# Performance work log

Measured on AMD Instinct MI355X. Metric: run time of the kernel, lower is better.

## Reference

```python
import jax, jax.numpy as jnp
import numpy as np
import math

IN_CH = 32
OUT_CH = 32
NODE_NUM = 24
BATCH = 32768
# skeleton edges: self-loops + chain (parent -> child), matching init_kwargs
_SRC = list(range(24)) + list(range(23))
_DST = list(range(24)) + list(range(1, 24))


def _build_mask():
    # block mask: block (dst, src) of size [OUT_CH, IN_CH] set to 1 per edge
    m = np.zeros((OUT_CH * NODE_NUM, IN_CH * NODE_NUM), dtype=np.float32)
    for s, d in zip(_SRC, _DST):
        m[OUT_CH * d:OUT_CH * (d + 1), IN_CH * s:IN_CH * (s + 1)] = 1.0
    return jnp.asarray(m)


def setup_inputs() -> dict:
    key = jax.random.key(0)
    kx, kw, kb = jax.random.split(key, 3)
    mask = _build_mask()
    dim = IN_CH * NODE_NUM
    # kaiming-uniform-like per-block init approximated by scaled normal; only
    # values inside mask blocks matter (forward multiplies by mask anyway)
    weight = jax.random.normal(kw, (OUT_CH * NODE_NUM, dim), dtype=jnp.float32) * (1.0 / math.sqrt(IN_CH))
    bound = 1.0 / math.sqrt(dim)
    bias = jax.random.uniform(kb, (OUT_CH * NODE_NUM,), dtype=jnp.float32, minval=-bound, maxval=bound)
    x = jax.random.normal(kx, (BATCH, dim), dtype=jnp.float32)
    return {"x": x, "weight": weight, "bias": bias, "mask": mask}


def reference(x, weight, bias, mask):
    # F.linear(x, weight * mask, bias) == x @ (weight*mask)^T + bias
    w = weight * mask
    return jnp.einsum("bi,oi->bo", x, w) + bias
```

## Files before the change

### kernel.cpp

```cpp
#include <hip/hip_runtime.h>
#include <hip/hip_bf16.h>


typedef __bf16 bf16x8 __attribute__((ext_vector_type(8)));
typedef float  f32x4  __attribute__((ext_vector_type(4)));

#define DIM 768
#define STRIDE 770
#define NFRAG (24 * 2 * 2)

__device__ __forceinline__ bf16x8 cvt8(const float* __restrict__ p) {
    float4 lo = *(const float4*)p;
    float4 hi = *(const float4*)(p + 4);
    bf16x8 r;
    r[0] = (__bf16)lo.x; r[1] = (__bf16)lo.y; r[2] = (__bf16)lo.z; r[3] = (__bf16)lo.w;
    r[4] = (__bf16)hi.x; r[5] = (__bf16)hi.y; r[6] = (__bf16)hi.z; r[7] = (__bf16)hi.w;
    return r;
}

__global__ void prepack_w_kernel(const float* __restrict__ w, bf16x8* __restrict__ ws)
{
    const int fid = blockIdx.x * 256 + threadIdx.x;
    const int lane = fid & 63;
    const int ni   = (fid >> 6) & 1;
    const int kt   = (fid >> 7) & 1;
    const int d    = fid >> 8;
    const int quad = lane >> 4, l16 = lane & 15;

    bf16x8 v;
    if (d == 0 && kt == 0) {
#pragma unroll
        for (int j = 0; j < 8; ++j) v[j] = (__bf16)0.f;
    } else {
        const float* src = w + (long)(32 * d + 16 * ni + l16) * DIM
                             + (32 * d - 32 + 32 * kt + 8 * quad);
        v = cvt8(src);
    }
    ws[fid] = v;
}

__global__ __launch_bounds__(512, 4)
void skeleton_linear_kernel(const float* __restrict__ x,
                            const float* __restrict__ bias,
                            const bf16x8* __restrict__ wfrag,
                            float* __restrict__ out)
{
    __shared__ float lds[16 * STRIDE];

    const int tid  = threadIdx.x;
    const int lane = tid & 63;
    const int wave = tid >> 6;
    const int quad = lane >> 4;
    const int l16  = lane & 15;
    const long row0 = (long)blockIdx.x * 16;

    {
        const float4* gx = (const float4*)(x + row0 * DIM);
        float4 st[6];
#pragma unroll
        for (int i = 0; i < 6; ++i) st[i] = gx[tid + 512 * i];
#pragma unroll
        for (int i = 0; i < 6; ++i) {
            int f = tid + 512 * i;
            int r = f / 192, c4 = f % 192;
            *(float4*)&lds[r * STRIDE + 4 * c4] = st[i];
        }
    }
    __syncthreads();

    f32x4 acc[3][2];
#pragma unroll
    for (int i = 0; i < 3; ++i) {
        const int d = wave * 3 + i;
        f32x4 a0 = {0.f, 0.f, 0.f, 0.f};
        f32x4 a1 = {0.f, 0.f, 0.f, 0.f};
#pragma unroll
        for (int kt = 0; kt < 2; ++kt) {
            int k0 = 32 * d - 32 + 32 * kt + 8 * quad;
            int kA = k0 < 0 ? 0 : k0;
            bf16x8 a = cvt8(&lds[l16 * STRIDE + kA]);
            const int fb = (d * 2 + kt) * 2;
            a0 = __builtin_amdgcn_mfma_f32_16x16x32_bf16(a, wfrag[fb * 64 + lane], a0, 0, 0, 0);
            a1 = __builtin_amdgcn_mfma_f32_16x16x32_bf16(a, wfrag[(fb + 1) * 64 + lane], a1, 0, 0, 0);
        }
        acc[i][0] = a0;
        acc[i][1] = a1;
    }
    __syncthreads();

#pragma unroll
    for (int i = 0; i < 3; ++i) {
        const int d = wave * 3 + i;
#pragma unroll
        for (int ni = 0; ni < 2; ++ni) {
            const float bi = bias[32 * d + 16 * ni + l16];
#pragma unroll
            for (int r = 0; r < 4; ++r)
                lds[(4 * quad + r) * STRIDE + 32 * d + 16 * ni + l16] = acc[i][ni][r] + bi;
        }
    }
    __syncthreads();

    {
        float* go = out + row0 * DIM;
#pragma unroll
        for (int i = 0; i < 6; ++i) {
            int f = tid + 512 * i;
            int r = f / 192, c4 = f % 192;
            float4 v = *(const float4*)&lds[r * STRIDE + 4 * c4];
            *(float4*)(go + (long)r * DIM + 4 * c4) = v;
        }
    }
}

extern "C" void kernel_launch(void* const* d_in, const int* in_sizes, int n_in,
                              void* d_out, int out_size, void* d_ws, size_t ws_size,
                              hipStream_t stream) {
    const float* x    = (const float*)d_in[0];
    const float* w    = (const float*)d_in[1];
    const float* bias = (const float*)d_in[2];
    float* out = (float*)d_out;

    bf16x8* wpack = (bf16x8*)d_ws;

    prepack_w_kernel<<<NFRAG * 64 / 256, 256, 0, stream>>>(w, wpack);

    const int BATCH = 32768;
    dim3 grid(BATCH / 16);
    skeleton_linear_kernel<<<grid, 512, 0, stream>>>(x, bias, wpack, out);
}
```

Baseline: 188.5 us.

## Load x straight into MFMA fragments and store outputs directly without LDS

Drops the LDS staging of x and of the output tile, along with its three block barriers. Each lane now loads its MFMA operand slices straight from global memory. The weight and activation operands are swapped so that each lane's accumulator holds four consecutive output channels, which lets it write a float4 directly to global memory. Bias is added by initialising the accumulators from it. The cost is that global loads and stores are less coalesced per instruction (strided rows, 32-byte and 16-byte chunks), traded for removing LDS traffic and synchronisation.

```diff
diff --git a/kernel.cpp b/kernel.cpp
--- a/kernel.cpp
+++ b/kernel.cpp
@@ -6,12 +6,18 @@
 typedef float  f32x4  __attribute__((ext_vector_type(4)));
 
 #define DIM 768
-#define STRIDE 770
 #define NFRAG (24 * 2 * 2)
 
 __device__ __forceinline__ bf16x8 cvt8(const float* __restrict__ p) {
     float4 lo = *(const float4*)p;
     float4 hi = *(const float4*)(p + 4);
+    bf16x8 r;
+    r[0] = (__bf16)lo.x; r[1] = (__bf16)lo.y; r[2] = (__bf16)lo.z; r[3] = (__bf16)lo.w;
+    r[4] = (__bf16)hi.x; r[5] = (__bf16)hi.y; r[6] = (__bf16)hi.z; r[7] = (__bf16)hi.w;
+    return r;
+}
+
+__device__ __forceinline__ bf16x8 cvt8r(float4 lo, float4 hi) {
     bf16x8 r;
     r[0] = (__bf16)lo.x; r[1] = (__bf16)lo.y; r[2] = (__bf16)lo.z; r[3] = (__bf16)lo.w;
     r[4] = (__bf16)hi.x; r[5] = (__bf16)hi.y; r[6] = (__bf16)hi.z; r[7] = (__bf16)hi.w;
@@ -45,71 +51,40 @@
                             const bf16x8* __restrict__ wfrag,
                             float* __restrict__ out)
 {
-    __shared__ float lds[16 * STRIDE];
-
     const int tid  = threadIdx.x;
     const int lane = tid & 63;
     const int wave = tid >> 6;
     const int quad = lane >> 4;
     const int l16  = lane & 15;
-    const long row0 = (long)blockIdx.x * 16;
+    const long row = (long)blockIdx.x * 16 + l16;
 
-    {
-        const float4* gx = (const float4*)(x + row0 * DIM);
-        float4 st[6];
+    const float* xr = x + row * DIM + 8 * quad;
+    float4 lo[4], hi[4];
 #pragma unroll
-        for (int i = 0; i < 6; ++i) st[i] = gx[tid + 512 * i];
+    for (int s = 0; s < 4; ++s) {
+        int kb = 32 * (3 * wave - 1 + s);
+        if (kb < 0) kb = 0;
+        lo[s] = *(const float4*)(xr + kb);
+        hi[s] = *(const float4*)(xr + kb + 4);
+    }
+    bf16x8 xf[4];
 #pragma unroll
-        for (int i = 0; i < 6; ++i) {
-            int f = tid + 512 * i;
-            int r = f / 192, c4 = f % 192;
-            *(float4*)&lds[r * STRIDE + 4 * c4] = st[i];
-        }
-    }
-    __syncthreads();
+    for (int s = 0; s < 4; ++s) xf[s] = cvt8r(lo[s], hi[s]);
 
-    f32x4 acc[3][2];
+    float* orow = out + row * DIM;
 #pragma unroll
     for (int i = 0; i < 3; ++i) {
-        const int d = wave * 3 + i;
-        f32x4 a0 = {0.f, 0.f, 0.f, 0.f};
-        f32x4 a1 = {0.f, 0.f, 0.f, 0.f};
+        const int d = 3 * wave + i;
+        f32x4 acc0 = *(const f32x4*)(bias + 32 * d + 4 * quad);
+        f32x4 acc1 = *(const f32x4*)(bias + 32 * d + 16 + 4 * quad);
 #pragma unroll
         for (int kt = 0; kt < 2; ++kt) {
-            int k0 = 32 * d - 32 + 32 * kt + 8 * quad;
-            int kA = k0 < 0 ? 0 : k0;
-            bf16x8 a = cvt8(&lds[l16 * STRIDE + kA]);
-            const int fb = (d * 2 + kt) * 2;
-            a0 = __builtin_amdgcn_mfma_f32_16x16x32_bf16(a, wfrag[fb * 64 + lane], a0, 0, 0, 0);
-            a1 = __builtin_amdgcn_mfma_f32_16x16x32_bf16(a, wfrag[(fb + 1) * 64 + lane], a1, 0, 0, 0);
+            const int fb = (d * 2 + kt) * 2 * 64 + lane;
+            acc0 = __builtin_amdgcn_mfma_f32_16x16x32_bf16(wfrag[fb],      xf[i + kt], acc0, 0, 0, 0);
+            acc1 = __builtin_amdgcn_mfma_f32_16x16x32_bf16(wfrag[fb + 64], xf[i + kt], acc1, 0, 0, 0);
         }
-        acc[i][0] = a0;
-        acc[i][1] = a1;
-    }
-    __syncthreads();
-
-#pragma unroll
-    for (int i = 0; i < 3; ++i) {
-        const int d = wave * 3 + i;
-#pragma unroll
-        for (int ni = 0; ni < 2; ++ni) {
-            const float bi = bias[32 * d + 16 * ni + l16];
-#pragma unroll
-            for (int r = 0; r < 4; ++r)
-                lds[(4 * quad + r) * STRIDE + 32 * d + 16 * ni + l16] = acc[i][ni][r] + bi;
-        }
-    }
-    __syncthreads();
-
-    {
-        float* go = out + row0 * DIM;
-#pragma unroll
-        for (int i = 0; i < 6; ++i) {
-            int f = tid + 512 * i;
-            int r = f / 192, c4 = f % 192;
-            float4 v = *(const float4*)&lds[r * STRIDE + 4 * c4];
-            *(float4*)(go + (long)r * DIM + 4 * c4) = v;
-        }
+        *(f32x4*)(orow + 32 * d + 4 * quad)      = acc0;
+        *(f32x4*)(orow + 32 * d + 16 + 4 * quad) = acc1;
     }
 }
 
```

Result: slower. 195.8 us (+3.8%).
